# Kernel optimization log

Hardware: AMD Instinct MI355X
Metric: run time of the kernel (lower is better)

The kernel has to match this reference:

```python
import jax, jax.numpy as jnp
import numpy as np

N_NODES = 50000
N_EDGES = 800000
NODE_F = 128
EDGE_F = 64
OUT_F = 128


def setup_inputs() -> dict:
    key = jax.random.key(0)
    k1, k2, k3, k4, k5 = jax.random.split(key, 5)
    x = jax.random.normal(k1, (N_NODES, NODE_F), dtype=jnp.float32)
    edge_index = jax.random.randint(k2, (2, N_EDGES), 0, N_NODES, dtype=jnp.int64)
    edge_attr = jax.random.normal(k3, (N_EDGES, EDGE_F), dtype=jnp.float32)
    # Linear(node_features + edge_features, out_features) params (torch default init scale)
    fan_in = NODE_F + EDGE_F
    bound = 1.0 / np.sqrt(fan_in)
    W = jax.random.uniform(k4, (fan_in, OUT_F), minval=-bound, maxval=bound, dtype=jnp.float32)
    b = jax.random.uniform(k5, (OUT_F,), minval=-bound, maxval=bound, dtype=jnp.float32)
    return {"x": x, "edge_index": edge_index, "edge_attr": edge_attr, "W": W, "b": b}


def reference(x, edge_index, edge_attr, W, b):
    # PyG source_to_target flow: x_j = x[src], aggregate at dst
    src = edge_index[0]
    dst = edge_index[1]
    x_j = x[src]                                   # [E, node_f] gather
    feats = jnp.concatenate([edge_attr, x_j], axis=1)  # [E, edge_f + node_f]
    msg = jax.nn.relu(feats @ W + b)               # [E, out_f] Linear + ReLU
    out = jax.ops.segment_sum(msg, dst, num_segments=x.shape[0])  # scatter-add
    return out
```

## Files before the change

### kernel.cpp

```cpp
#include <hip/hip_runtime.h>
#include <hip/hip_bf16.h>

#define N_NODES 50000
#define N_EDGES 800000
#define NODE_F  128
#define EDGE_F  64
#define OUT_F   128
#define K_DIM   192
#define TILE_M  32
#define LDS_STRIDE 200
#define N_TILES (N_EDGES / TILE_M)
#define NBLOCKS 2048

typedef __attribute__((ext_vector_type(8))) short short8;
typedef __attribute__((ext_vector_type(4))) short short4v;
typedef __attribute__((ext_vector_type(4))) float floatx4;

__device__ __forceinline__ unsigned short f2bf(float f) {
    unsigned int u = __float_as_uint(f);
    u += 0x7fffu + ((u >> 16) & 1u);
    return (unsigned short)(u >> 16);
}

__global__ __launch_bounds__(256, 4) void gnn_branch_kernel(
    const float* __restrict__ x,
    const int*   __restrict__ edge_index,
    const float* __restrict__ edge_attr,
    const float* __restrict__ W,
    const float* __restrict__ bias,
    float*       __restrict__ out)
{
    __shared__ __align__(16) unsigned short feats[TILE_M][LDS_STRIDE];
    __shared__ int dst_lds[TILE_M];

    const int tid  = threadIdx.x;
    const int wave = tid >> 6;
    const int lane = tid & 63;
    const int col  = lane & 15;
    const int quad = lane >> 4;
    const int wbase = wave * 32;

    short8 bfr[6][2];
    #pragma unroll
    for (int kc = 0; kc < 6; ++kc) {
        #pragma unroll
        for (int ns = 0; ns < 2; ++ns) {
            const int n    = wbase + ns * 16 + col;
            const int krow = kc * 32 + quad * 8;
            short8 v;
            #pragma unroll
            for (int j = 0; j < 8; ++j)
                v[j] = (short)f2bf(W[(krow + j) * OUT_F + n]);
            bfr[kc][ns] = v;
        }
    }
    const float b0 = bias[wbase + col];
    const float b1 = bias[wbase + 16 + col];

    const int* __restrict__ srcp = edge_index;
    const int* __restrict__ dstp = edge_index + N_EDGES;

    for (int tile = blockIdx.x; tile < N_TILES; tile += gridDim.x) {
        const int e0 = tile * TILE_M;

        if (tid < TILE_M) dst_lds[tid] = dstp[e0 + tid];

        {
            const int e   = tid >> 3;
            const int sub = tid & 7;
            const int src = srcp[e0 + e];
            const float* __restrict__ ea = edge_attr + (size_t)(e0 + e) * EDGE_F;
            const float* __restrict__ xr = x + (size_t)src * NODE_F;
            #pragma unroll
            for (int i = 0; i < 6; ++i) {
                const int fi = sub + 8 * i;
                floatx4 v;
                if (fi < 16) v = *(const floatx4*)(ea + fi * 4);
                else         v = *(const floatx4*)(xr + (fi - 16) * 4);
                short4v sv;
                sv[0] = (short)f2bf(v[0]);
                sv[1] = (short)f2bf(v[1]);
                sv[2] = (short)f2bf(v[2]);
                sv[3] = (short)f2bf(v[3]);
                *(short4v*)&feats[e][fi * 4] = sv;
            }
        }
        __syncthreads();

        floatx4 acc[2][2] = {};
        #pragma unroll
        for (int kc = 0; kc < 6; ++kc) {
            short8 a0 = *(const short8*)&feats[col     ][kc * 32 + quad * 8];
            short8 a1 = *(const short8*)&feats[16 + col][kc * 32 + quad * 8];
            acc[0][0] = __builtin_amdgcn_mfma_f32_16x16x32_bf16(a0, bfr[kc][0], acc[0][0], 0, 0, 0);
            acc[0][1] = __builtin_amdgcn_mfma_f32_16x16x32_bf16(a0, bfr[kc][1], acc[0][1], 0, 0, 0);
            acc[1][0] = __builtin_amdgcn_mfma_f32_16x16x32_bf16(a1, bfr[kc][0], acc[1][0], 0, 0, 0);
            acc[1][1] = __builtin_amdgcn_mfma_f32_16x16x32_bf16(a1, bfr[kc][1], acc[1][1], 0, 0, 0);
        }

        #pragma unroll
        for (int ms = 0; ms < 2; ++ms) {
            #pragma unroll
            for (int r = 0; r < 4; ++r) {
                const int m = ms * 16 + quad * 4 + r;
                const int d = dst_lds[m];
                float* orow = out + (size_t)d * OUT_F + wbase;
                const float v0 = acc[ms][0][r] + b0;
                const float v1 = acc[ms][1][r] + b1;
                if (v0 > 0.0f) atomicAdd(orow + col,      v0);
                if (v1 > 0.0f) atomicAdd(orow + 16 + col, v1);
            }
        }
        __syncthreads();
    }
}

extern "C" void kernel_launch(void* const* d_in, const int* in_sizes, int n_in,
                              void* d_out, int out_size, void* d_ws, size_t ws_size,
                              hipStream_t stream) {
    const float* x          = (const float*)d_in[0];
    const int*   edge_index = (const int*)  d_in[1];
    const float* edge_attr  = (const float*)d_in[2];
    const float* W          = (const float*)d_in[3];
    const float* bias       = (const float*)d_in[4];
    float*       out        = (float*)d_out;

    hipMemsetAsync(out, 0, (size_t)out_size * sizeof(float), stream);

    gnn_branch_kernel<<<dim3(NBLOCKS), dim3(256), 0, stream>>>(
        x, edge_index, edge_attr, W, bias, out);
}
```

Measured before the change: 560.4 us.

## Precompute per-node x@W projection, then gather projected rows in edge kernel

```diff
diff --git a/kernel.cpp b/kernel.cpp
--- a/kernel.cpp
+++ b/kernel.cpp
@@ -6,11 +6,6 @@
 #define NODE_F  128
 #define EDGE_F  64
 #define OUT_F   128
-#define K_DIM   192
-#define TILE_M  32
-#define LDS_STRIDE 200
-#define N_TILES (N_EDGES / TILE_M)
-#define NBLOCKS 2048
 
 typedef __attribute__((ext_vector_type(8))) short short8;
 typedef __attribute__((ext_vector_type(4))) short short4v;
@@ -22,16 +17,17 @@
     return (unsigned short)(u >> 16);
 }
 
-__global__ __launch_bounds__(256, 4) void gnn_branch_kernel(
+#define TILE_N1 32
+#define N_NTILES ((N_NODES + TILE_N1 - 1) / TILE_N1)
+#define LDS_STRIDE1 136
+
+__global__ __launch_bounds__(256, 4) void node_kernel(
     const float* __restrict__ x,
-    const int*   __restrict__ edge_index,
-    const float* __restrict__ edge_attr,
     const float* __restrict__ W,
     const float* __restrict__ bias,
-    float*       __restrict__ out)
+    float*       __restrict__ Y)
 {
-    __shared__ __align__(16) unsigned short feats[TILE_M][LDS_STRIDE];
-    __shared__ int dst_lds[TILE_M];
+    __shared__ __align__(16) unsigned short xs[TILE_N1][LDS_STRIDE1];
 
     const int tid  = threadIdx.x;
     const int wave = tid >> 6;
@@ -40,58 +36,53 @@
     const int quad = lane >> 4;
     const int wbase = wave * 32;
 
-    short8 bfr[6][2];
+    const float* __restrict__ Wx = W + EDGE_F * OUT_F;
+
+    short8 bfr[4][2];
     #pragma unroll
-    for (int kc = 0; kc < 6; ++kc) {
+    for (int kc = 0; kc < 4; ++kc) {
         #pragma unroll
         for (int ns = 0; ns < 2; ++ns) {
-            const int n    = wbase + ns * 16 + col;
+            const int n = wbase + ns * 16 + col;
             const int krow = kc * 32 + quad * 8;
             short8 v;
             #pragma unroll
             for (int j = 0; j < 8; ++j)
-                v[j] = (short)f2bf(W[(krow + j) * OUT_F + n]);
+                v[j] = (short)f2bf(Wx[(krow + j) * OUT_F + n]);
             bfr[kc][ns] = v;
         }
     }
     const float b0 = bias[wbase + col];
     const float b1 = bias[wbase + 16 + col];
 
-    const int* __restrict__ srcp = edge_index;
-    const int* __restrict__ dstp = edge_index + N_EDGES;
-
-    for (int tile = blockIdx.x; tile < N_TILES; tile += gridDim.x) {
-        const int e0 = tile * TILE_M;
-
-        if (tid < TILE_M) dst_lds[tid] = dstp[e0 + tid];
+    for (int tile = blockIdx.x; tile < N_NTILES; tile += gridDim.x) {
+        const int n0 = tile * TILE_N1;
 
         {
             const int e   = tid >> 3;
             const int sub = tid & 7;
-            const int src = srcp[e0 + e];
-            const float* __restrict__ ea = edge_attr + (size_t)(e0 + e) * EDGE_F;
-            const float* __restrict__ xr = x + (size_t)src * NODE_F;
-            #pragma unroll
-            for (int i = 0; i < 6; ++i) {
+            const int node = n0 + e;
+            const float* __restrict__ xr = x + (size_t)node * NODE_F;
+            #pragma unroll
+            for (int i = 0; i < 4; ++i) {
                 const int fi = sub + 8 * i;
-                floatx4 v;
-                if (fi < 16) v = *(const floatx4*)(ea + fi * 4);
-                else         v = *(const floatx4*)(xr + (fi - 16) * 4);
+                floatx4 v = {0.f, 0.f, 0.f, 0.f};
+                if (node < N_NODES) v = *(const floatx4*)(xr + fi * 4);
                 short4v sv;
                 sv[0] = (short)f2bf(v[0]);
                 sv[1] = (short)f2bf(v[1]);
                 sv[2] = (short)f2bf(v[2]);
                 sv[3] = (short)f2bf(v[3]);
-                *(short4v*)&feats[e][fi * 4] = sv;
+                *(short4v*)&xs[e][fi * 4] = sv;
             }
         }
         __syncthreads();
 
         floatx4 acc[2][2] = {};
         #pragma unroll
-        for (int kc = 0; kc < 6; ++kc) {
-            short8 a0 = *(const short8*)&feats[col     ][kc * 32 + quad * 8];
-            short8 a1 = *(const short8*)&feats[16 + col][kc * 32 + quad * 8];
+        for (int kc = 0; kc < 4; ++kc) {
+            short8 a0 = *(const short8*)&xs[col     ][kc * 32 + quad * 8];
+            short8 a1 = *(const short8*)&xs[16 + col][kc * 32 + quad * 8];
             acc[0][0] = __builtin_amdgcn_mfma_f32_16x16x32_bf16(a0, bfr[kc][0], acc[0][0], 0, 0, 0);
             acc[0][1] = __builtin_amdgcn_mfma_f32_16x16x32_bf16(a0, bfr[kc][1], acc[0][1], 0, 0, 0);
             acc[1][0] = __builtin_amdgcn_mfma_f32_16x16x32_bf16(a1, bfr[kc][0], acc[1][0], 0, 0, 0);
@@ -103,15 +94,102 @@
             #pragma unroll
             for (int r = 0; r < 4; ++r) {
                 const int m = ms * 16 + quad * 4 + r;
-                const int d = dst_lds[m];
-                float* orow = out + (size_t)d * OUT_F + wbase;
-                const float v0 = acc[ms][0][r] + b0;
-                const float v1 = acc[ms][1][r] + b1;
-                if (v0 > 0.0f) atomicAdd(orow + col,      v0);
-                if (v1 > 0.0f) atomicAdd(orow + 16 + col, v1);
+                const int node = n0 + m;
+                if (node < N_NODES) {
+                    float* yrow = Y + (size_t)node * OUT_F + wbase;
+                    yrow[col]      = acc[ms][0][r] + b0;
+                    yrow[16 + col] = acc[ms][1][r] + b1;
+                }
             }
         }
         __syncthreads();
+    }
+}
+
+#define TILE_E   16
+#define N_ETILES (N_EDGES / TILE_E)
+#define NBLOCKS2 1024
+
+__global__ __launch_bounds__(256, 3) void edge_kernel(
+    const float* __restrict__ edge_attr,
+    const int*   __restrict__ edge_index,
+    const float* __restrict__ W,
+    const float* __restrict__ Y,
+    float*       __restrict__ out)
+{
+    const int lane = threadIdx.x & 63;
+    const int col  = lane & 15;
+    const int quad = lane >> 4;
+
+    short8 bfr[2][8];
+    #pragma unroll
+    for (int kc = 0; kc < 2; ++kc) {
+        #pragma unroll
+        for (int ns = 0; ns < 8; ++ns) {
+            const int n = ns * 16 + col;
+            const int krow = kc * 32 + quad * 8;
+            short8 v;
+            #pragma unroll
+            for (int j = 0; j < 8; ++j)
+                v[j] = (short)f2bf(W[(krow + j) * OUT_F + n]);
+            bfr[kc][ns] = v;
+        }
+    }
+
+    const int* __restrict__ srcp = edge_index;
+    const int* __restrict__ dstp = edge_index + N_EDGES;
+
+    const int gwave  = blockIdx.x * 4 + (threadIdx.x >> 6);
+    const int nwaves = gridDim.x * 4;
+
+    for (int t = gwave; t < N_ETILES; t += nwaves) {
+        const int e0 = t * TILE_E;
+
+        const float* __restrict__ ar = edge_attr + (size_t)(e0 + col) * EDGE_F;
+        short8 a[2];
+        #pragma unroll
+        for (int kc = 0; kc < 2; ++kc) {
+            floatx4 v0 = *(const floatx4*)(ar + kc * 32 + quad * 8);
+            floatx4 v1 = *(const floatx4*)(ar + kc * 32 + quad * 8 + 4);
+            short8 av;
+            av[0] = (short)f2bf(v0[0]); av[1] = (short)f2bf(v0[1]);
+            av[2] = (short)f2bf(v0[2]); av[3] = (short)f2bf(v0[3]);
+            av[4] = (short)f2bf(v1[0]); av[5] = (short)f2bf(v1[1]);
+            av[6] = (short)f2bf(v1[2]); av[7] = (short)f2bf(v1[3]);
+            a[kc] = av;
+        }
+
+        int sr[4], dr[4];
+        #pragma unroll
+        for (int r = 0; r < 4; ++r) {
+            sr[r] = srcp[e0 + quad * 4 + r];
+            dr[r] = dstp[e0 + quad * 4 + r];
+        }
+
+        floatx4 acc[8];
+        #pragma unroll
+        for (int ns = 0; ns < 8; ++ns) {
+            #pragma unroll
+            for (int r = 0; r < 4; ++r)
+                acc[ns][r] = Y[(size_t)sr[r] * OUT_F + ns * 16 + col];
+        }
+
+        #pragma unroll
+        for (int kc = 0; kc < 2; ++kc) {
+            #pragma unroll
+            for (int ns = 0; ns < 8; ++ns)
+                acc[ns] = __builtin_amdgcn_mfma_f32_16x16x32_bf16(a[kc], bfr[kc][ns], acc[ns], 0, 0, 0);
+        }
+
+        #pragma unroll
+        for (int ns = 0; ns < 8; ++ns) {
+            #pragma unroll
+            for (int r = 0; r < 4; ++r) {
+                const float v = acc[ns][r];
+                if (v > 0.0f)
+                    atomicAdd(out + (size_t)dr[r] * OUT_F + ns * 16 + col, v);
+            }
+        }
     }
 }
 
@@ -124,9 +202,10 @@
     const float* W          = (const float*)d_in[3];
     const float* bias       = (const float*)d_in[4];
     float*       out        = (float*)d_out;
+    float*       Y          = (float*)d_ws;
 
     hipMemsetAsync(out, 0, (size_t)out_size * sizeof(float), stream);
 
-    gnn_branch_kernel<<<dim3(NBLOCKS), dim3(256), 0, stream>>>(
-        x, edge_index, edge_attr, W, bias, out);
-}
+    node_kernel<<<dim3(512), dim3(256), 0, stream>>>(x, W, bias, Y);
+    edge_kernel<<<dim3(NBLOCKS2), dim3(256), 0, stream>>>(edge_attr, edge_index, W, Y, out);
+}
```

Measured after the change: 578.9 us. 3.3% more time.
